# Optimization experiments

Measured on AMD Instinct MI355X. Metric: run time of the kernel, lower is better.

## Reference

```python
import jax, jax.numpy as jnp
from jax import lax
import numpy as np

BN_EPS = 1e-5  # nn.BatchNorm2d default eps (eval mode with running stats)


def setup_inputs() -> dict:
    key = jax.random.key(0)
    ks = jax.random.split(key, 6)
    B, C, O, H, W = 4, 64, 64, 128, 128
    x = jax.random.normal(ks[0], (B, C, H, W), jnp.float32)
    # conv_offset: 27 = 3 * deform_groups * kh * kw output channels, zero-bias.
    # Scaled small to mimic the near-zero init of ModulatedDeformConv2dPack.
    w_off = jax.random.normal(ks[1], (27, C, 3, 3), jnp.float32) * 0.05
    b_off = jnp.zeros((27,), jnp.float32)
    weight = jax.random.normal(ks[2], (O, C, 3, 3), jnp.float32) * (1.0 / np.sqrt(C * 9))
    bias = jax.random.normal(ks[3], (O,), jnp.float32) * 0.1
    gamma = jax.random.normal(ks[4], (O,), jnp.float32) * 0.1 + 1.0
    beta = jax.random.normal(ks[5], (O,), jnp.float32) * 0.1
    running_mean = jnp.zeros((O,), jnp.float32)
    running_var = jnp.ones((O,), jnp.float32)
    return {"x": x, "w_off": w_off, "b_off": b_off, "weight": weight, "bias": bias,
            "gamma": gamma, "beta": beta, "running_mean": running_mean, "running_var": running_var}


def _dcn_bn_relu(x, w_off, b_off, weight, bias, gamma, beta, running_mean, running_var):
    B, C, H, W = x.shape
    O = weight.shape[0]
    K = 9  # 3x3 kernel taps
    # --- offset/mask conv (regular 3x3, stride 1, pad 1) ---
    off = lax.conv_general_dilated(x, w_off, (1, 1), ((1, 1), (1, 1)),
                                   dimension_numbers=("NCHW", "OIHW", "NCHW"))
    off = off + b_off[None, :, None, None]
    o1, o2, m = jnp.split(off, 3, axis=1)  # each [B,9,H,W]
    # mmcv layout: cat(o1,o2) then interpreted as (tap, [y,x]) pairs
    offset = jnp.concatenate([o1, o2], axis=1).reshape(B, K, 2, H, W)
    mask = jax.nn.sigmoid(m)  # [B,K,H,W]
    # --- sampling grid: p = (h - pad + i*dil + dy, w - pad + j*dil + dx) ---
    ky = (jnp.repeat(jnp.arange(3), 3) - 1).astype(x.dtype)  # [K]
    kx = (jnp.tile(jnp.arange(3), 3) - 1).astype(x.dtype)
    py = jnp.arange(H, dtype=x.dtype)[None, None, :, None] + ky[None, :, None, None] + offset[:, :, 0]
    px = jnp.arange(W, dtype=x.dtype)[None, None, None, :] + kx[None, :, None, None] + offset[:, :, 1]
    y0 = jnp.floor(py); x0 = jnp.floor(px)
    dy = py - y0; dx = px - x0  # [B,K,H,W]
    y0i = y0.astype(jnp.int32); x0i = x0.astype(jnp.int32)

    def gather(yi, xi):
        # zero outside bounds (mmcv bilinear semantics)
        valid = (yi >= 0) & (yi < H) & (xi >= 0) & (xi < W)
        yc = jnp.clip(yi, 0, H - 1)
        xc = jnp.clip(xi, 0, W - 1)
        g = jax.vmap(lambda xb, yb, xb2: xb[:, yb, xb2])(x, yc, xc)  # [B,C,K,H,W]
        return g * valid[:, None].astype(x.dtype)

    w00 = ((1 - dy) * (1 - dx))[:, None]
    w01 = ((1 - dy) * dx)[:, None]
    w10 = (dy * (1 - dx))[:, None]
    w11 = (dy * dx)[:, None]
    samp = (gather(y0i, x0i) * w00 + gather(y0i, x0i + 1) * w01 +
            gather(y0i + 1, x0i) * w10 + gather(y0i + 1, x0i + 1) * w11)
    samp = samp * mask[:, None]  # modulation, [B,C,K,H,W]
    # conv accumulation over (channel, tap)
    out = jnp.einsum("ock,bckhw->bohw", weight.reshape(O, C, K), samp)
    out = out + bias[None, :, None, None]
    # --- BatchNorm2d (eval, running stats) + ReLU ---
    scale = gamma / jnp.sqrt(running_var + BN_EPS)
    out = (out - running_mean[None, :, None, None]) * scale[None, :, None, None] + beta[None, :, None, None]
    return jax.nn.relu(out)


def reference(x, w_off, b_off, weight, bias, gamma, beta, running_mean, running_var):
    return _dcn_bn_relu(x, w_off, b_off, weight, bias, gamma, beta, running_mean, running_var)
```

## Files before the change

### kernel.cpp

```cpp
#include <hip/hip_runtime.h>
#include <hip/hip_bf16.h>


#define HH 128
#define WW 128
#define KP2 200

typedef __attribute__((ext_vector_type(8))) short bf16x8;
typedef __attribute__((ext_vector_type(4))) float f32x4;

__device__ __forceinline__ unsigned short f2bf(float f) {
    union { __hip_bfloat16 b; unsigned short u; } cv;
    cv.b = __float2bfloat16(f);
    return cv.u;
}
__device__ __forceinline__ float bf2f(unsigned short u) {
    union { unsigned int i; float f; } cv;
    cv.i = ((unsigned int)u) << 16;
    return cv.f;
}

#define WBM_ELEMS 36864
#define WBO_ELEMS 18432
#define XT_OFF    55296

__global__ __launch_bounds__(256) void transpose_kernel(
    const float* __restrict__ x,
    const float* __restrict__ w_off,
    const float* __restrict__ wgt,
    unsigned short* __restrict__ ws)
{
    __shared__ float tile[64 * 65];
    const int tid = threadIdx.x;

    {
        int t = blockIdx.x * 256 + tid;
        if (t < WBM_ELEMS) {
            int j = t & 7, lane = (t >> 3) & 63, nt = (t >> 9) & 3, kb = t >> 11;
            int k = kb * 32 + ((lane >> 4) << 3) + j;
            int n = nt * 16 + (lane & 15);
            int tap = k >> 6, c = k & 63;
            ws[t] = f2bf(wgt[n * 576 + c * 9 + tap]);
        } else if (t < WBM_ELEMS + WBO_ELEMS) {
            int t2 = t - WBM_ELEMS;
            int j = t2 & 7, lane = (t2 >> 3) & 63, nt = (t2 >> 9) & 1, kb = t2 >> 10;
            int k = kb * 32 + ((lane >> 4) << 3) + j;
            int n = nt * 16 + (lane & 15);
            int tap = k >> 6, c = k & 63;
            ws[t] = (n < 27) ? f2bf(w_off[n * 576 + c * 9 + tap]) : (unsigned short)0;
        }
    }

    const int bb  = blockIdx.x >> 8;
    const int hw0 = (blockIdx.x & 255) << 6;
    const float* xb = x + ((size_t)bb << 20);
#pragma unroll
    for (int it = 0; it < 16; ++it) {
        int idx = it * 256 + tid;
        int c = idx >> 6, i = idx & 63;
        tile[c * 65 + i] = xb[(c << 14) + hw0 + i];
    }
    __syncthreads();
    unsigned int* xtb = (unsigned int*)(ws + XT_OFF) + ((size_t)bb << 19);
#pragma unroll
    for (int it = 0; it < 8; ++it) {
        int idx = it * 256 + tid;
        int i = idx >> 5, c2 = idx & 31;
        unsigned int lo = (unsigned int)f2bf(tile[(2 * c2) * 65 + i]);
        unsigned int hi = (unsigned int)f2bf(tile[(2 * c2 + 1) * 65 + i]);
        xtb[(size_t)(hw0 + i) * 32 + c2] = lo | (hi << 16);
    }
}

__global__ __launch_bounds__(256) void DeformConv_14568529068723_kernel(
    const float* __restrict__ b_off,
    const float* __restrict__ bias,
    const float* __restrict__ gamma,
    const float* __restrict__ beta,
    const float* __restrict__ rmean,
    const float* __restrict__ rvar,
    const unsigned short* __restrict__ ws,
    float* __restrict__ out)
{
    __shared__ __align__(16) unsigned short samp[32 * KP2];
    __shared__ float eL[4][9][32];
    __shared__ int   oL[2][9][32];
    __shared__ float sbuf[176];

    const int tid  = threadIdx.x;
    const int wv   = tid >> 6;
    const int lane = tid & 63;
    const int px16 = lane & 15;
    const int cg   = lane >> 4;
    const int c8   = tid & 7;
    const int pxq  = tid >> 3;

    if (tid < 64) {
        float sc = gamma[tid] * __frsqrt_rn(rvar[tid] + 1e-5f);
        sbuf[tid] = sc;
        sbuf[64 + tid] = (bias[tid] - rmean[tid]) * sc + beta[tid];
        if (tid < 27) sbuf[128 + tid] = b_off[tid];
    }

    const int bid = blockIdx.x;
    const int swz = ((bid & 7) << 8) + (bid >> 3);
    const int p0   = swz * 32;
    const int b    = p0 >> 14;
    const int rem0 = p0 & 16383;
    const int h    = rem0 >> 7;
    const int w0   = rem0 & 127;
    const unsigned short* xt = ws + XT_OFF + ((size_t)b << 20);

    const bf16x8* WbM = (const bf16x8*)ws;
    const bf16x8* WbO = (const bf16x8*)(ws + WBM_ELEMS);

    __syncthreads();

    const int mtO = wv >> 1;
    const int ocO = wv & 1;
    f32x4 accO = (f32x4){0.f, 0.f, 0.f, 0.f};

    for (int chk = 0; chk < 3; ++chk) {
#pragma unroll
        for (int tl = 0; tl < 3; ++tl) {
            int tap = chk * 3 + tl;
            int ky = tap / 3 - 1, kx = tap % 3 - 1;
            int yy = h + ky;
            int yc = min(max(yy, 0), HH - 1);
            bool oky = (yy >= 0) & (yy < HH);
            int xx = w0 + pxq + kx;
            bool ok = oky & (xx >= 0) & (xx < WW);
            int pos = yc * WW + min(max(xx, 0), WW - 1);
            uint4 v = *(const uint4*)(xt + pos * 64 + (c8 << 3));
            if (!ok) { v.x = 0u; v.y = 0u; v.z = 0u; v.w = 0u; }
            *(uint4*)&samp[pxq * KP2 + tl * 64 + (c8 << 3)] = v;
        }
        __syncthreads();
#pragma unroll
        for (int st = 0; st < 6; ++st) {
            int kb = chk * 6 + st;
            bf16x8 bO = WbO[(kb * 2 + ocO) * 64 + lane];
            bf16x8 af = *(const bf16x8*)&samp[(mtO * 16 + px16) * KP2 + st * 32 + (cg << 3)];
            accO = __builtin_amdgcn_mfma_f32_16x16x32_bf16(af, bO, accO, 0, 0, 0);
        }
        __syncthreads();
    }
    float* offs = (float*)samp;
    {
        int n0 = ocO * 16 + (lane & 15);
        int mB = cg * 4;
#pragma unroll
        for (int r = 0; r < 4; ++r) {
            int pxc = mtO * 16 + mB + r;
            if (n0 < 27) {
                float vv = accO[r] + sbuf[128 + n0];
                if (n0 >= 18) vv = 1.0f / (1.0f + __expf(-vv));
                offs[n0 * 32 + pxc] = vv;
            }
        }
    }
    __syncthreads();

#pragma unroll
    for (int base = 0; base < 288; base += 256) {
        int idx = base + tid;
        if (idx < 288) {
            int px = idx & 31, tap = idx >> 5;
            float o1 = offs[(2 * tap) * 32 + px];
            float o2 = offs[(2 * tap + 1) * 32 + px];
            float m  = offs[(18 + tap) * 32 + px];
            float py  = (float)(h + tap / 3 - 1) + o1;
            float pxf = (float)(w0 + px + tap % 3 - 1) + o2;
            float y0f = floorf(py), x0f = floorf(pxf);
            float dy = py - y0f, dx = pxf - x0f;
            int y0 = (int)y0f, x0 = (int)x0f;
            int y1 = y0 + 1, x1 = x0 + 1;
            int yc0 = min(max(y0, 0), HH - 1), yc1 = min(max(y1, 0), HH - 1);
            int xc0 = min(max(x0, 0), WW - 1), xc1 = min(max(x1, 0), WW - 1);
            float vy0 = (y0 >= 0 && y0 < HH) ? 1.0f : 0.0f;
            float vy1 = (y1 >= 0 && y1 < HH) ? 1.0f : 0.0f;
            float vx0 = (x0 >= 0 && x0 < WW) ? 1.0f : 0.0f;
            float vx1 = (x1 >= 0 && x1 < WW) ? 1.0f : 0.0f;
            float c00 = (1.0f - dy) * (1.0f - dx) * m * vy0 * vx0;
            float c01 = (1.0f - dy) * dx * m * vy0 * vx1;
            float c10 = dy * (1.0f - dx) * m * vy1 * vx0;
            float c11 = dy * dx * m * vy1 * vx1;
            int bx = min(xc0, WW - 2);
            bool s0 = (xc0 != bx), s1 = (xc1 != bx);
            eL[0][tap][px] = (s0 ? 0.f : c00) + (s1 ? 0.f : c01);
            eL[1][tap][px] = (s0 ? c00 : 0.f) + (s1 ? c01 : 0.f);
            eL[2][tap][px] = (s0 ? 0.f : c10) + (s1 ? 0.f : c11);
            eL[3][tap][px] = (s0 ? c10 : 0.f) + (s1 ? c11 : 0.f);
            oL[0][tap][px] = (yc0 * WW + bx) * 64;
            oL[1][tap][px] = (yc1 * WW + bx) * 64;
        }
    }
    __syncthreads();

    f32x4 acc[2];
#pragma unroll
    for (int mt = 0; mt < 2; ++mt) acc[mt] = (f32x4){0.f, 0.f, 0.f, 0.f};

    for (int chk = 0; chk < 3; ++chk) {
#pragma unroll
        for (int tl = 0; tl < 3; ++tl) {
            int tap = chk * 3 + tl;
            int o0 = oL[0][tap][pxq], o1r = oL[1][tap][pxq];
            float e0 = eL[0][tap][pxq], e1 = eL[1][tap][pxq];
            float e2 = eL[2][tap][pxq], e3 = eL[3][tap][pxq];
            uint4 a0 = *(const uint4*)(xt + o0 + (c8 << 3));
            uint4 a1 = *(const uint4*)(xt + o0 + 64 + (c8 << 3));
            uint4 b0 = *(const uint4*)(xt + o1r + (c8 << 3));
            uint4 b1 = *(const uint4*)(xt + o1r + 64 + (c8 << 3));
            const unsigned int* pa0 = (const unsigned int*)&a0;
            const unsigned int* pa1 = (const unsigned int*)&a1;
            const unsigned int* pb0 = (const unsigned int*)&b0;
            const unsigned int* pb1 = (const unsigned int*)&b1;
            uint4 pk;
            unsigned int* pp = (unsigned int*)&pk;
#pragma unroll
            for (int q = 0; q < 4; ++q) {
                float lo = e0 * bf2f((unsigned short)(pa0[q] & 0xffff))
                         + e1 * bf2f((unsigned short)(pa1[q] & 0xffff))
                         + e2 * bf2f((unsigned short)(pb0[q] & 0xffff))
                         + e3 * bf2f((unsigned short)(pb1[q] & 0xffff));
                float hi = e0 * bf2f((unsigned short)(pa0[q] >> 16))
                         + e1 * bf2f((unsigned short)(pa1[q] >> 16))
                         + e2 * bf2f((unsigned short)(pb0[q] >> 16))
                         + e3 * bf2f((unsigned short)(pb1[q] >> 16));
                pp[q] = (unsigned int)f2bf(lo) | ((unsigned int)f2bf(hi) << 16);
            }
            *(uint4*)&samp[pxq * KP2 + tl * 64 + (c8 << 3)] = pk;
        }
        __syncthreads();
#pragma unroll
        for (int st = 0; st < 6; ++st) {
            int kb = chk * 6 + st;
            bf16x8 bf = WbM[(kb * 4 + wv) * 64 + lane];
            bf16x8 af0 = *(const bf16x8*)&samp[px16 * KP2 + st * 32 + (cg << 3)];
            bf16x8 af1 = *(const bf16x8*)&samp[(16 + px16) * KP2 + st * 32 + (cg << 3)];
            acc[0] = __builtin_amdgcn_mfma_f32_16x16x32_bf16(af0, bf, acc[0], 0, 0, 0);
            acc[1] = __builtin_amdgcn_mfma_f32_16x16x32_bf16(af1, bf, acc[1], 0, 0, 0);
        }
        __syncthreads();
    }

    float* dT = (float*)samp;
    {
        int n0 = lane & 15;
        int mB = cg * 4;
#pragma unroll
        for (int mt = 0; mt < 2; ++mt)
#pragma unroll
            for (int r = 0; r < 4; ++r)
                dT[(wv * 16 + n0) * 33 + mt * 16 + mB + r] = acc[mt][r];
    }
    __syncthreads();
    {
        int px = tid & 31;
        int oh = tid >> 5;
#pragma unroll
        for (int i = 0; i < 8; ++i) {
            int o = 8 * i + oh;
            float v = dT[o * 33 + px];
            v = fmaxf(fmaf(v, sbuf[o], sbuf[64 + o]), 0.0f);
            out[(((size_t)(b * 64 + o)) << 14) + rem0 + px] = v;
        }
    }
}

extern "C" void kernel_launch(void* const* d_in, const int* in_sizes, int n_in,
                              void* d_out, int out_size, void* d_ws, size_t ws_size,
                              hipStream_t stream) {
    (void)in_sizes; (void)n_in; (void)ws_size; (void)out_size;
    const float* x     = (const float*)d_in[0];
    const float* w_off = (const float*)d_in[1];
    const float* b_off = (const float*)d_in[2];
    const float* wgt   = (const float*)d_in[3];
    const float* bias  = (const float*)d_in[4];
    const float* gamma = (const float*)d_in[5];
    const float* beta  = (const float*)d_in[6];
    const float* rmean = (const float*)d_in[7];
    const float* rvar  = (const float*)d_in[8];
    unsigned short* wsB = (unsigned short*)d_ws;
    float* outp = (float*)d_out;

    transpose_kernel<<<dim3(1024), dim3(256), 0, stream>>>(x, w_off, wgt, wsB);
    DeformConv_14568529068723_kernel<<<dim3(2048), dim3(256), 0, stream>>>(
        b_off, bias, gamma, beta, rmean, rvar, wsB, outp);
}
```

Measured before the change: 113.3 us.

## Stage one halo row per kernel row for offset conv with swizzled LDS

The offset-conv stage used to gather three shifted 32-pixel copies per kernel row into shared memory. It now loads a single 34-column halo row per kernel row into a buffer that reuses the eL shared array, with an XOR swizzle to avoid bank conflicts. The three horizontal taps are then read at shifted column offsets. This cuts global loads and LDS writes by about three times. The MFMA work now runs on only two waves, each doing two M-tiles, so the other two waves sit idle during this phase.

Result: no change. 112.0 us (-1.2%).

```diff
diff --git a/kernel.cpp b/kernel.cpp
--- a/kernel.cpp
+++ b/kernel.cpp
@@ -83,7 +83,7 @@
     float* __restrict__ out)
 {
     __shared__ __align__(16) unsigned short samp[32 * KP2];
-    __shared__ float eL[4][9][32];
+    __shared__ __align__(16) float eL[4][9][32];
     __shared__ int   oL[2][9][32];
     __shared__ float sbuf[176];
 
@@ -114,49 +114,61 @@
     const bf16x8* WbM = (const bf16x8*)ws;
     const bf16x8* WbO = (const bf16x8*)(ws + WBM_ELEMS);
 
-    __syncthreads();
-
-    const int mtO = wv >> 1;
-    const int ocO = wv & 1;
-    f32x4 accO = (f32x4){0.f, 0.f, 0.f, 0.f};
+    unsigned short* rowbuf = (unsigned short*)eL;
+
+    __syncthreads();
+
+    f32x4 accO[2];
+#pragma unroll
+    for (int q = 0; q < 2; ++q) accO[q] = (f32x4){0.f, 0.f, 0.f, 0.f};
 
     for (int chk = 0; chk < 3; ++chk) {
-#pragma unroll
-        for (int tl = 0; tl < 3; ++tl) {
-            int tap = chk * 3 + tl;
-            int ky = tap / 3 - 1, kx = tap % 3 - 1;
-            int yy = h + ky;
+        {
+            int yy = h + chk - 1;
             int yc = min(max(yy, 0), HH - 1);
             bool oky = (yy >= 0) & (yy < HH);
-            int xx = w0 + pxq + kx;
-            bool ok = oky & (xx >= 0) & (xx < WW);
-            int pos = yc * WW + min(max(xx, 0), WW - 1);
-            uint4 v = *(const uint4*)(xt + pos * 64 + (c8 << 3));
-            if (!ok) { v.x = 0u; v.y = 0u; v.z = 0u; v.w = 0u; }
-            *(uint4*)&samp[pxq * KP2 + tl * 64 + (c8 << 3)] = v;
+            for (int i = tid; i < 272; i += 256) {
+                int cc = i >> 3, c8i = i & 7;
+                int gx = w0 - 1 + cc;
+                bool ok = oky & (gx >= 0) & (gx < WW);
+                int xc = min(max(gx, 0), WW - 1);
+                uint4 v = *(const uint4*)(xt + (yc * WW + xc) * 64 + (c8i << 3));
+                if (!ok) { v.x = 0u; v.y = 0u; v.z = 0u; v.w = 0u; }
+                *(uint4*)&rowbuf[(cc * 64) + (((c8i ^ (cc & 7)) << 3))] = v;
+            }
         }
         __syncthreads();
-#pragma unroll
-        for (int st = 0; st < 6; ++st) {
-            int kb = chk * 6 + st;
-            bf16x8 bO = WbO[(kb * 2 + ocO) * 64 + lane];
-            bf16x8 af = *(const bf16x8*)&samp[(mtO * 16 + px16) * KP2 + st * 32 + (cg << 3)];
-            accO = __builtin_amdgcn_mfma_f32_16x16x32_bf16(af, bO, accO, 0, 0, 0);
+        if (wv < 2) {
+#pragma unroll
+            for (int st = 0; st < 6; ++st) {
+                int kb = chk * 6 + st;
+                int tl = st >> 1;
+                int g0 = (st & 1) * 4 + cg;
+                bf16x8 bO = WbO[(kb * 2 + wv) * 64 + lane];
+#pragma unroll
+                for (int mt = 0; mt < 2; ++mt) {
+                    int col = mt * 16 + px16 + tl;
+                    bf16x8 af = *(const bf16x8*)&rowbuf[(col * 64) + (((g0 ^ (col & 7)) << 3))];
+                    accO[mt] = __builtin_amdgcn_mfma_f32_16x16x32_bf16(af, bO, accO[mt], 0, 0, 0);
+                }
+            }
         }
         __syncthreads();
     }
     float* offs = (float*)samp;
-    {
-        int n0 = ocO * 16 + (lane & 15);
+    if (wv < 2) {
+        int n0 = wv * 16 + (lane & 15);
         int mB = cg * 4;
-#pragma unroll
-        for (int r = 0; r < 4; ++r) {
-            int pxc = mtO * 16 + mB + r;
-            if (n0 < 27) {
-                float vv = accO[r] + sbuf[128 + n0];
-                if (n0 >= 18) vv = 1.0f / (1.0f + __expf(-vv));
-                offs[n0 * 32 + pxc] = vv;
-            }
+        if (n0 < 27) {
+#pragma unroll
+            for (int mt = 0; mt < 2; ++mt)
+#pragma unroll
+                for (int r = 0; r < 4; ++r) {
+                    int pxc = mt * 16 + mB + r;
+                    float vv = accO[mt][r] + sbuf[128 + n0];
+                    if (n0 >= 18) vv = 1.0f / (1.0f + __expf(-vv));
+                    offs[n0 * 32 + pxc] = vv;
+                }
         }
     }
     __syncthreads();
```
